# Kernel tuning notes

Hardware: AMD Instinct MI355X
Metric: run time of the kernel (lower is better)

## Reference

```python
import jax, jax.numpy as jnp
import numpy as np

BATCH = 8192
N = 32
A_NUM = 5
EPS = 1e-10
ALPHA = jnp.array([0.01, 0.25, 0.5, 0.9, 0.99], dtype=jnp.float32)


def setup_inputs() -> dict:
    key = jax.random.key(0)
    ks = jax.random.split(key, 9)
    stdv = 1.0 / np.sqrt(N)
    u = lambda k, shape: jax.random.uniform(k, shape, jnp.float32, -stdv, stdv)
    L = N * (N - 1) // 2
    return {
        "inputs": jax.random.normal(ks[0], (BATCH, N, N), jnp.float32),
        "state": jax.random.normal(ks[1], (BATCH, A_NUM * N * N), jnp.float32),
        "WR_root": u(ks[2], (A_NUM,)),
        "Wt_root": u(ks[3], (1,)),
        "Wphi_root": u(ks[4], (1,)),
        "Ws_root": u(ks[5], (A_NUM,)),
        "Br": u(ks[6], (L, 1)),
        "Bt": u(ks[7], (L, 1)),
        "By": u(ks[8], (L, 1)),
    }


def _skew(Bvec, n):
    # Replicates the torch loop: row 0 is zeros; row k (k>=1) gets B[k-1 : 2k-1]
    # in its first k columns (overlapping slices of the flat parameter vector).
    b = Bvec.reshape(-1)
    r = jnp.arange(n)[:, None]
    c = jnp.arange(n)[None, :]
    idx = jnp.clip(r - 1 + c, 0, b.shape[0] - 1)  # B[k-1+j] for entry (k, j)
    L = jnp.where(c < r, b[idx], jnp.zeros((), b.dtype))
    return L - L.T


def _cayley(S, n):
    # MatrixExp in the source: (I - S)^{-1} (I + S)
    I = jnp.eye(n, dtype=S.dtype)
    return jnp.linalg.solve(I - S, I + S)


def _translate(A, Bvec, n):
    # M @ A @ M.T with M the Cayley 'exp' of the skew matrix built from Bvec.
    M = _cayley(_skew(Bvec, n), n)
    return jnp.einsum('ij,bjk,lk->bil', M, A, M)


def _nus(W_root, A, eps):
    # Weighted average over the a_num axis with weights W_root^2 / (sum + eps).
    W = W_root * W_root
    return jnp.einsum('a,banm->bnm', W / (W.sum() + eps), A)


def reference(inputs, state, WR_root, Wt_root, Wphi_root, Ws_root, Br, Bt, By):
    Mt_1 = state.reshape(-1, A_NUM, N, N)                 # [B, a, n, n]
    X = inputs.reshape(BATCH, N, N)                       # [B, n, n]

    Yt = _nus(WR_root, Mt_1, EPS)                         # [B, n, n]
    Rt = _translate(Yt, Br, N)

    at = (Wt_root[0] ** 2) / ((Wt_root ** 2 + Wphi_root ** 2).sum() + EPS)
    Tt = (1.0 - at) * X + at * Rt                         # Frechet mean FM
    Phit = _translate(Tt, Bt, N)

    # Per-j Frechet means, vectorized over the a_num axis.
    a = ALPHA[None, :, None, None]
    Mt = (1.0 - a) * Mt_1 + a * Phit[:, None, :, :]       # [B, a, n, n]

    St = _nus(Ws_root, Mt, EPS)
    Ot = _translate(St, By, N)                            # [B, n, n]

    return Ot, Mt.reshape(-1, A_NUM, N, N)
```

## Files before the change

kernel.cpp:

```cpp
#include <hip/hip_runtime.h>

#define NB 8192
#define OT_ELEMS (NB * 1024)
#define EPSF 1e-10f

typedef __attribute__((ext_vector_type(4))) float f32x4;
typedef __attribute__((ext_vector_type(8))) short s16x8;

#define SBAR() __builtin_amdgcn_sched_barrier(0)
#define LGK()  do { SBAR(); asm volatile("s_waitcnt lgkmcnt(0)"); SBAR(); } while (0)

#define MFMA_B16(A, B, C) __builtin_amdgcn_mfma_f32_16x16x32_bf16((A), (B), (C), 0, 0, 0)

__global__ void cayley_kernel(const float* __restrict__ Br,
                              const float* __restrict__ Bt,
                              const float* __restrict__ By,
                              float* __restrict__ M_out) {
  __shared__ float A[32][33];
  __shared__ float R[32][33];
  const float* B = (blockIdx.x == 0) ? Br : (blockIdx.x == 1) ? Bt : By;
  const int t = threadIdx.x;
  const int i = t >> 5, j = t & 31;
  float Lij = (j < i) ? B[i - 1 + j] : 0.0f;
  float Lji = (i < j) ? B[j - 1 + i] : 0.0f;
  float S = Lij - Lji;
  float eye = (i == j) ? 1.0f : 0.0f;
  A[i][j] = eye - S;
  R[i][j] = eye + S;
  __syncthreads();
  for (int p = 0; p < 32; ++p) {
    float f = A[i][p] / A[p][p];
    __syncthreads();
    if (i != p) {
      A[i][j] -= f * A[p][j];
      R[i][j] -= f * R[p][j];
    }
    __syncthreads();
  }
  M_out[blockIdx.x * 1024 + i * 32 + j] = R[i][j] / A[i][i];
}

__global__ void combine_kernel(float* __restrict__ ws) {
  __shared__ float sMR[1024], sMT[1024];
  const int t = threadIdx.x;
  sMR[t] = ws[t];
  sMT[t] = ws[1024 + t];
  __syncthreads();
  const int i = t >> 5, j = t & 31;
  float s = 0.f;
#pragma unroll
  for (int k = 0; k < 32; ++k)
    s = fmaf(sMT[i * 32 + k], sMR[k * 32 + j], s);
  ws[3072 + i * 32 + j] = s;
}

__device__ __forceinline__ void cvt_hilo8(const f32x4 f0, const f32x4 f1, s16x8& hi, s16x8& lo) {
  float f[8];
#pragma unroll
  for (int e = 0; e < 4; ++e) { f[e] = f0[e]; f[4 + e] = f1[e]; }
#pragma unroll
  for (int e = 0; e < 8; ++e) {
    unsigned u = __float_as_uint(f[e]);
    hi[e] = (short)(u >> 16);
    float ah = __uint_as_float(u & 0xffff0000u);
    lo[e] = (short)(__float_as_uint(f[e] - ah) >> 16);
  }
}

__device__ __forceinline__ void read_frag_lds(const float* sb, int off, s16x8& hi, s16x8& lo) {
  f32x4 f0 = *(const f32x4*)(sb + off);
  f32x4 f1 = *(const f32x4*)(sb + off + 4);
  cvt_hilo8(f0, f1, hi, lo);
}

__global__ __launch_bounds__(64) void spdsru_main(
    const float* __restrict__ X, const float* __restrict__ state,
    const float* __restrict__ WR, const float* __restrict__ Wt,
    const float* __restrict__ Wphi, const float* __restrict__ Ws,
    const float* __restrict__ Mg, float* __restrict__ out) {
  __shared__ __align__(16) float sb0[1184];
  __shared__ __align__(16) float sb1[1184];
  const int lane = threadIdx.x;
  const int l15 = lane & 15, l4 = lane >> 4;
  const int i0 = (lane >> 3) << 2, j0 = (lane & 7) << 2;
  const int bid = blockIdx.x;
  const int batch = (bid & 7) * (NB >> 3) + (bid >> 3);

  s16x8 Mh[3][2], Ml[3][2];
  {
    const int srcoff[3] = {1024, 3072, 2048};
#pragma unroll
    for (int q = 0; q < 3; ++q)
#pragma unroll
      for (int s = 0; s < 2; ++s) {
        const float* p = Mg + srcoff[q] + (16 * s + l15) * 32 + 8 * l4;
        cvt_hilo8(*(const f32x4*)p, *(const f32x4*)(p + 4), Mh[q][s], Ml[q][s]);
      }
  }

  const float alpha[5] = {0.01f, 0.25f, 0.5f, 0.9f, 0.99f};
  float wr[5], va[5];
  float cP = 0.f;
  {
    float sR = 0.f, sS = 0.f, wq[5];
#pragma unroll
    for (int a = 0; a < 5; ++a) { float v = WR[a]; wr[a] = v * v; sR += v * v; }
#pragma unroll
    for (int a = 0; a < 5; ++a) { float v = Ws[a]; wq[a] = v * v; sS += v * v; }
    const float invR = 1.0f / (sR + EPSF), invS = 1.0f / (sS + EPSF);
#pragma unroll
    for (int a = 0; a < 5; ++a) {
      wr[a] *= invR;
      float w = wq[a] * invS;
      va[a] = w * (1.0f - alpha[a]);
      cP += w * alpha[a];
    }
  }
  const float wt2 = Wt[0] * Wt[0], wp2 = Wphi[0] * Wphi[0];
  const float at = wt2 / (wt2 + wp2 + EPSF);
  const float omat = 1.0f - at;

  const float* xp = X + (size_t)batch * 1024;
  f32x4 x[4];
#pragma unroll
  for (int r = 0; r < 4; ++r)
    x[r] = __builtin_nontemporal_load((const f32x4*)(xp + (i0 + r) * 32 + j0));

  const float* stp = state + (size_t)batch * 5120;
  f32x4 U[4], V[4];
#pragma unroll
  for (int r = 0; r < 4; ++r) { U[r] = f32x4{0.f, 0.f, 0.f, 0.f}; V[r] = U[r]; }
#pragma unroll
  for (int a = 0; a < 5; ++a)
#pragma unroll
    for (int r = 0; r < 4; ++r) {
      const f32x4 v = *(const f32x4*)(stp + a * 1024 + (i0 + r) * 32 + j0);
      U[r] += wr[a] * v;
      V[r] += va[a] * v;
    }

#pragma unroll
  for (int c = 0; c < 4; ++c) {
    f32x4 cx = {x[0][c], x[1][c], x[2][c], x[3][c]};
    f32x4 cu = {U[0][c], U[1][c], U[2][c], U[3][c]};
    *(f32x4*)(sb0 + (j0 + c) * 36 + i0) = cx;
    *(f32x4*)(sb1 + (j0 + c) * 36 + i0) = cu;
  }
  LGK();
  s16x8 BXh[2], BXl[2], BUh[2], BUl[2];
#pragma unroll
  for (int s = 0; s < 2; ++s) {
    read_frag_lds(sb0, (16 * s + l15) * 36 + 8 * l4, BXh[s], BXl[s]);
    read_frag_lds(sb1, (16 * s + l15) * 36 + 8 * l4, BUh[s], BUl[s]);
  }
  LGK();
  f32x4 gX[2][2], gU[2][2];
#pragma unroll
  for (int ms = 0; ms < 2; ++ms)
#pragma unroll
    for (int ns = 0; ns < 2; ++ns) {
      f32x4 a0 = {0.f, 0.f, 0.f, 0.f};
      a0 = MFMA_B16(Ml[0][ms], BXh[ns], a0);
      a0 = MFMA_B16(Mh[0][ms], BXl[ns], a0);
      a0 = MFMA_B16(Mh[0][ms], BXh[ns], a0);
      gX[ms][ns] = a0;
      f32x4 a1 = {0.f, 0.f, 0.f, 0.f};
      a1 = MFMA_B16(Ml[1][ms], BUh[ns], a1);
      a1 = MFMA_B16(Mh[1][ms], BUl[ns], a1);
      a1 = MFMA_B16(Mh[1][ms], BUh[ns], a1);
      gU[ms][ns] = a1;
    }
#pragma unroll
  for (int ms = 0; ms < 2; ++ms)
#pragma unroll
    for (int ns = 0; ns < 2; ++ns)
#pragma unroll
      for (int r = 0; r < 4; ++r) {
        sb0[(16 * ms + 4 * l4 + r) * 36 + 16 * ns + l15] = gX[ms][ns][r];
        sb1[(16 * ms + 4 * l4 + r) * 36 + 16 * ns + l15] = gU[ms][ns][r];
      }
  LGK();
  s16x8 AXh[2], AXl[2], AUh[2], AUl[2];
#pragma unroll
  for (int s = 0; s < 2; ++s) {
    read_frag_lds(sb0, (16 * s + l15) * 36 + 8 * l4, AXh[s], AXl[s]);
    read_frag_lds(sb1, (16 * s + l15) * 36 + 8 * l4, AUh[s], AUl[s]);
  }
  LGK();
  f32x4 ph[2][2];
#pragma unroll
  for (int ms = 0; ms < 2; ++ms)
#pragma unroll
    for (int ns = 0; ns < 2; ++ns) {
      f32x4 a0 = {0.f, 0.f, 0.f, 0.f};
      a0 = MFMA_B16(AXl[ms], Mh[0][ns], a0);
      a0 = MFMA_B16(AXh[ms], Ml[0][ns], a0);
      a0 = MFMA_B16(AXh[ms], Mh[0][ns], a0);
      f32x4 a1 = {0.f, 0.f, 0.f, 0.f};
      a1 = MFMA_B16(AUl[ms], Mh[1][ns], a1);
      a1 = MFMA_B16(AUh[ms], Ml[1][ns], a1);
      a1 = MFMA_B16(AUh[ms], Mh[1][ns], a1);
      ph[ms][ns] = omat * a0 + at * a1;
    }

#pragma unroll
  for (int ms = 0; ms < 2; ++ms)
#pragma unroll
    for (int ns = 0; ns < 2; ++ns)
#pragma unroll
      for (int r = 0; r < 4; ++r)
        sb0[(16 * ms + 4 * l4 + r) * 36 + 16 * ns + l15] = ph[ms][ns][r];
  LGK();
  f32x4 ph4[4];
#pragma unroll
  for (int r = 0; r < 4; ++r)
    ph4[r] = *(const f32x4*)(sb0 + (i0 + r) * 36 + j0);
  LGK();

  f32x4 st4[4];
#pragma unroll
  for (int r = 0; r < 4; ++r) st4[r] = V[r] + cP * ph4[r];
#pragma unroll
  for (int c = 0; c < 4; ++c) {
    f32x4 cs = {st4[0][c], st4[1][c], st4[2][c], st4[3][c]};
    *(f32x4*)(sb0 + (j0 + c) * 36 + i0) = cs;
  }
  f32x4 raw[20];
#pragma unroll
  for (int a = 0; a < 5; ++a)
#pragma unroll
    for (int r = 0; r < 4; ++r)
      raw[a * 4 + r] = *(const f32x4*)(stp + a * 1024 + (i0 + r) * 32 + j0);
  LGK();

  s16x8 BSh[2], BSl[2];
#pragma unroll
  for (int s = 0; s < 2; ++s)
    read_frag_lds(sb0, (16 * s + l15) * 36 + 8 * l4, BSh[s], BSl[s]);
  LGK();
  f32x4 gS[2][2];
#pragma unroll
  for (int ms = 0; ms < 2; ++ms)
#pragma unroll
    for (int ns = 0; ns < 2; ++ns) {
      f32x4 acc = {0.f, 0.f, 0.f, 0.f};
      acc = MFMA_B16(Ml[2][ms], BSh[ns], acc);
      acc = MFMA_B16(Mh[2][ms], BSl[ns], acc);
      acc = MFMA_B16(Mh[2][ms], BSh[ns], acc);
      gS[ms][ns] = acc;
    }
  float* outMt = out + OT_ELEMS + (size_t)batch * 5120;
#pragma unroll
  for (int a = 0; a < 5; ++a) {
    const float al = alpha[a], om = 1.0f - al;
#pragma unroll
    for (int r = 0; r < 4; ++r) {
      f32x4 w = om * raw[a * 4 + r] + al * ph4[r];
      __builtin_nontemporal_store(w, (f32x4*)(outMt + a * 1024 + (i0 + r) * 32 + j0));
    }
  }
#pragma unroll
  for (int ms = 0; ms < 2; ++ms)
#pragma unroll
    for (int ns = 0; ns < 2; ++ns)
#pragma unroll
      for (int r = 0; r < 4; ++r)
        sb0[(16 * ms + 4 * l4 + r) * 36 + 16 * ns + l15] = gS[ms][ns][r];
  LGK();
  s16x8 ASh[2], ASl[2];
#pragma unroll
  for (int s = 0; s < 2; ++s)
    read_frag_lds(sb0, (16 * s + l15) * 36 + 8 * l4, ASh[s], ASl[s]);
  LGK();
  f32x4 o[2][2];
#pragma unroll
  for (int ms = 0; ms < 2; ++ms)
#pragma unroll
    for (int ns = 0; ns < 2; ++ns) {
      f32x4 acc = {0.f, 0.f, 0.f, 0.f};
      acc = MFMA_B16(ASl[ms], Mh[2][ns], acc);
      acc = MFMA_B16(ASh[ms], Ml[2][ns], acc);
      acc = MFMA_B16(ASh[ms], Mh[2][ns], acc);
      o[ms][ns] = acc;
    }
#pragma unroll
  for (int ms = 0; ms < 2; ++ms)
#pragma unroll
    for (int ns = 0; ns < 2; ++ns)
#pragma unroll
      for (int r = 0; r < 4; ++r)
        sb0[(16 * ms + 4 * l4 + r) * 36 + 16 * ns + l15] = o[ms][ns][r];
  LGK();
  float* outOt = out + (size_t)batch * 1024;
#pragma unroll
  for (int r = 0; r < 4; ++r) {
    f32x4 ov = *(const f32x4*)(sb0 + (i0 + r) * 36 + j0);
    __builtin_nontemporal_store(ov, (f32x4*)(outOt + (i0 + r) * 32 + j0));
  }
}

extern "C" void kernel_launch(void* const* d_in, const int* in_sizes, int n_in,
                              void* d_out, int out_size, void* d_ws, size_t ws_size,
                              hipStream_t stream) {
  const float* X     = (const float*)d_in[0];
  const float* state = (const float*)d_in[1];
  const float* WR    = (const float*)d_in[2];
  const float* Wt    = (const float*)d_in[3];
  const float* Wphi  = (const float*)d_in[4];
  const float* Ws    = (const float*)d_in[5];
  const float* Br    = (const float*)d_in[6];
  const float* Bt    = (const float*)d_in[7];
  const float* By    = (const float*)d_in[8];
  float* m_ws = (float*)d_ws;
  float* outp = (float*)d_out;

  cayley_kernel<<<3, 1024, 0, stream>>>(Br, Bt, By, m_ws);
  combine_kernel<<<1, 1024, 0, stream>>>(m_ws);
  spdsru_main<<<NB, 64, 0, stream>>>(X, state, WR, Wt, Wphi, Ws, m_ws, outp);
}
```

Baseline: 89.09 us.

## Precompose Cayley matrix products to flatten the dependent matmul chain

The combine kernel now also precomputes My*Mt and My*Mt*Mr, so the final output Ot is expressed directly as My·V·My^T + cP·omat·(MyMt)X(MyMt)^T + cP·at·(MyMtMr)U(...)^T. This removes the serial Phi→St→Ot stage and its LDS round trips, so all five first-stage products can be issued together and then all second-stage products. The state is loaded once into registers and reused for the Mt output instead of being reloaded. In exchange it does more MFMA work (five sandwich products instead of four), uses more LDS buffers and registers (which may lower occupancy), and changes the rounding behaviour of the bf16 hi/lo split.

```diff
diff --git a/kernel.cpp b/kernel.cpp
--- a/kernel.cpp
+++ b/kernel.cpp
@@ -41,17 +41,28 @@
 }
 
 __global__ void combine_kernel(float* __restrict__ ws) {
-  __shared__ float sMR[1024], sMT[1024];
+  __shared__ float sMR[1024], sMT[1024], sMY[1024], sP[1024];
   const int t = threadIdx.x;
   sMR[t] = ws[t];
   sMT[t] = ws[1024 + t];
+  sMY[t] = ws[2048 + t];
   __syncthreads();
   const int i = t >> 5, j = t & 31;
-  float s = 0.f;
+  float p = 0.f, q1 = 0.f;
+#pragma unroll
+  for (int k = 0; k < 32; ++k) {
+    p  = fmaf(sMT[i * 32 + k], sMR[k * 32 + j], p);
+    q1 = fmaf(sMY[i * 32 + k], sMT[k * 32 + j], q1);
+  }
+  sP[i * 32 + j] = p;
+  ws[3072 + i * 32 + j] = p;
+  ws[4096 + i * 32 + j] = q1;
+  __syncthreads();
+  float q2 = 0.f;
 #pragma unroll
   for (int k = 0; k < 32; ++k)
-    s = fmaf(sMT[i * 32 + k], sMR[k * 32 + j], s);
-  ws[3072 + i * 32 + j] = s;
+    q2 = fmaf(sMY[i * 32 + k], sP[k * 32 + j], q2);
+  ws[5120 + i * 32 + j] = q2;
 }
 
 __device__ __forceinline__ void cvt_hilo8(const f32x4 f0, const f32x4 f1, s16x8& hi, s16x8& lo) {
@@ -73,24 +84,30 @@
   cvt_hilo8(f0, f1, hi, lo);
 }
 
+#define PROD3(ACC, MH, ML, BH, BL)             \
+  do {                                         \
+    ACC = MFMA_B16((ML), (BH), ACC);           \
+    ACC = MFMA_B16((MH), (BL), ACC);           \
+    ACC = MFMA_B16((MH), (BH), ACC);           \
+  } while (0)
+
 __global__ __launch_bounds__(64) void spdsru_main(
     const float* __restrict__ X, const float* __restrict__ state,
     const float* __restrict__ WR, const float* __restrict__ Wt,
     const float* __restrict__ Wphi, const float* __restrict__ Ws,
     const float* __restrict__ Mg, float* __restrict__ out) {
-  __shared__ __align__(16) float sb0[1184];
-  __shared__ __align__(16) float sb1[1184];
+  __shared__ __align__(16) float sb0[1184], sb1[1184], sb2[1184], sb3[1184], sb4[1184];
   const int lane = threadIdx.x;
   const int l15 = lane & 15, l4 = lane >> 4;
   const int i0 = (lane >> 3) << 2, j0 = (lane & 7) << 2;
   const int bid = blockIdx.x;
   const int batch = (bid & 7) * (NB >> 3) + (bid >> 3);
 
-  s16x8 Mh[3][2], Ml[3][2];
+  s16x8 Mh[5][2], Ml[5][2];
   {
-    const int srcoff[3] = {1024, 3072, 2048};
-#pragma unroll
-    for (int q = 0; q < 3; ++q)
+    const int srcoff[5] = {1024, 3072, 2048, 4096, 5120};
+#pragma unroll
+    for (int q = 0; q < 5; ++q)
 #pragma unroll
       for (int s = 0; s < 2; ++s) {
         const float* p = Mg + srcoff[q] + (16 * s + l15) * 32 + 8 * l4;
@@ -119,184 +136,151 @@
   const float wt2 = Wt[0] * Wt[0], wp2 = Wphi[0] * Wphi[0];
   const float at = wt2 / (wt2 + wp2 + EPSF);
   const float omat = 1.0f - at;
-
+  const float cpo = cP * omat, cpa = cP * at;
+
+  const float* stp = state + (size_t)batch * 5120;
+  f32x4 m[5][4];
+#pragma unroll
+  for (int a = 0; a < 5; ++a)
+#pragma unroll
+    for (int r = 0; r < 4; ++r)
+      m[a][r] = *(const f32x4*)(stp + a * 1024 + (i0 + r) * 32 + j0);
   const float* xp = X + (size_t)batch * 1024;
   f32x4 x[4];
 #pragma unroll
   for (int r = 0; r < 4; ++r)
     x[r] = __builtin_nontemporal_load((const f32x4*)(xp + (i0 + r) * 32 + j0));
 
-  const float* stp = state + (size_t)batch * 5120;
   f32x4 U[4], V[4];
 #pragma unroll
-  for (int r = 0; r < 4; ++r) { U[r] = f32x4{0.f, 0.f, 0.f, 0.f}; V[r] = U[r]; }
-#pragma unroll
-  for (int a = 0; a < 5; ++a)
-#pragma unroll
-    for (int r = 0; r < 4; ++r) {
-      const f32x4 v = *(const f32x4*)(stp + a * 1024 + (i0 + r) * 32 + j0);
-      U[r] += wr[a] * v;
-      V[r] += va[a] * v;
-    }
+  for (int r = 0; r < 4; ++r) {
+    f32x4 u = wr[0] * m[0][r], v = va[0] * m[0][r];
+#pragma unroll
+    for (int a = 1; a < 5; ++a) { u += wr[a] * m[a][r]; v += va[a] * m[a][r]; }
+    U[r] = u; V[r] = v;
+  }
 
 #pragma unroll
   for (int c = 0; c < 4; ++c) {
     f32x4 cx = {x[0][c], x[1][c], x[2][c], x[3][c]};
     f32x4 cu = {U[0][c], U[1][c], U[2][c], U[3][c]};
+    f32x4 cv = {V[0][c], V[1][c], V[2][c], V[3][c]};
     *(f32x4*)(sb0 + (j0 + c) * 36 + i0) = cx;
     *(f32x4*)(sb1 + (j0 + c) * 36 + i0) = cu;
-  }
-  LGK();
-  s16x8 BXh[2], BXl[2], BUh[2], BUl[2];
+    *(f32x4*)(sb2 + (j0 + c) * 36 + i0) = cv;
+  }
+  LGK();
+
+  s16x8 BXh[2], BXl[2], BUh[2], BUl[2], BVh[2], BVl[2];
 #pragma unroll
   for (int s = 0; s < 2; ++s) {
     read_frag_lds(sb0, (16 * s + l15) * 36 + 8 * l4, BXh[s], BXl[s]);
     read_frag_lds(sb1, (16 * s + l15) * 36 + 8 * l4, BUh[s], BUl[s]);
-  }
-  LGK();
-  f32x4 gX[2][2], gU[2][2];
+    read_frag_lds(sb2, (16 * s + l15) * 36 + 8 * l4, BVh[s], BVl[s]);
+  }
+  LGK();
+
+#define STAGE_G(SB, G)                                                      \
+  do {                                                                      \
+    _Pragma("unroll") for (int ms = 0; ms < 2; ++ms)                        \
+      _Pragma("unroll") for (int ns = 0; ns < 2; ++ns)                      \
+        _Pragma("unroll") for (int r = 0; r < 4; ++r)                       \
+          (SB)[(16 * ms + 4 * l4 + r) * 36 + 16 * ns + l15] = G[ms][ns][r]; \
+  } while (0)
+
+  {
+    f32x4 g[2][2];
+#pragma unroll
+    for (int ms = 0; ms < 2; ++ms)
+#pragma unroll
+      for (int ns = 0; ns < 2; ++ns) { f32x4 a = {0,0,0,0}; PROD3(a, Mh[0][ms], Ml[0][ms], BXh[ns], BXl[ns]); g[ms][ns] = a; }
+    STAGE_G(sb0, g);
+#pragma unroll
+    for (int ms = 0; ms < 2; ++ms)
+#pragma unroll
+      for (int ns = 0; ns < 2; ++ns) { f32x4 a = {0,0,0,0}; PROD3(a, Mh[1][ms], Ml[1][ms], BUh[ns], BUl[ns]); g[ms][ns] = a; }
+    STAGE_G(sb1, g);
+#pragma unroll
+    for (int ms = 0; ms < 2; ++ms)
+#pragma unroll
+      for (int ns = 0; ns < 2; ++ns) { f32x4 a = {0,0,0,0}; PROD3(a, Mh[2][ms], Ml[2][ms], BVh[ns], BVl[ns]); g[ms][ns] = a; }
+    STAGE_G(sb2, g);
+#pragma unroll
+    for (int ms = 0; ms < 2; ++ms)
+#pragma unroll
+      for (int ns = 0; ns < 2; ++ns) { f32x4 a = {0,0,0,0}; PROD3(a, Mh[3][ms], Ml[3][ms], BXh[ns], BXl[ns]); g[ms][ns] = a; }
+    STAGE_G(sb3, g);
+#pragma unroll
+    for (int ms = 0; ms < 2; ++ms)
+#pragma unroll
+      for (int ns = 0; ns < 2; ++ns) { f32x4 a = {0,0,0,0}; PROD3(a, Mh[4][ms], Ml[4][ms], BUh[ns], BUl[ns]); g[ms][ns] = a; }
+    STAGE_G(sb4, g);
+  }
+  LGK();
+
+  s16x8 A1h[2], A1l[2], A2h[2], A2l[2];
+#pragma unroll
+  for (int s = 0; s < 2; ++s) {
+    read_frag_lds(sb0, (16 * s + l15) * 36 + 8 * l4, A1h[s], A1l[s]);
+    read_frag_lds(sb1, (16 * s + l15) * 36 + 8 * l4, A2h[s], A2l[s]);
+  }
+  LGK();
+
+  f32x4 ph[2][2];
 #pragma unroll
   for (int ms = 0; ms < 2; ++ms)
 #pragma unroll
     for (int ns = 0; ns < 2; ++ns) {
-      f32x4 a0 = {0.f, 0.f, 0.f, 0.f};
-      a0 = MFMA_B16(Ml[0][ms], BXh[ns], a0);
-      a0 = MFMA_B16(Mh[0][ms], BXl[ns], a0);
-      a0 = MFMA_B16(Mh[0][ms], BXh[ns], a0);
-      gX[ms][ns] = a0;
-      f32x4 a1 = {0.f, 0.f, 0.f, 0.f};
-      a1 = MFMA_B16(Ml[1][ms], BUh[ns], a1);
-      a1 = MFMA_B16(Mh[1][ms], BUl[ns], a1);
-      a1 = MFMA_B16(Mh[1][ms], BUh[ns], a1);
-      gU[ms][ns] = a1;
-    }
+      f32x4 a0 = {0,0,0,0}, a1 = {0,0,0,0};
+      PROD3(a0, A1h[ms], A1l[ms], Mh[0][ns], Ml[0][ns]);
+      PROD3(a1, A2h[ms], A2l[ms], Mh[1][ns], Ml[1][ns]);
+      ph[ms][ns] = omat * a0 + at * a1;
+    }
+  s16x8 A3h[2], A3l[2], A4h[2], A4l[2], A5h[2], A5l[2];
+#pragma unroll
+  for (int s = 0; s < 2; ++s) {
+    read_frag_lds(sb2, (16 * s + l15) * 36 + 8 * l4, A3h[s], A3l[s]);
+    read_frag_lds(sb3, (16 * s + l15) * 36 + 8 * l4, A4h[s], A4l[s]);
+    read_frag_lds(sb4, (16 * s + l15) * 36 + 8 * l4, A5h[s], A5l[s]);
+  }
+  LGK();
+
+  f32x4 ot[2][2];
 #pragma unroll
   for (int ms = 0; ms < 2; ++ms)
 #pragma unroll
-    for (int ns = 0; ns < 2; ++ns)
-#pragma unroll
-      for (int r = 0; r < 4; ++r) {
-        sb0[(16 * ms + 4 * l4 + r) * 36 + 16 * ns + l15] = gX[ms][ns][r];
-        sb1[(16 * ms + 4 * l4 + r) * 36 + 16 * ns + l15] = gU[ms][ns][r];
-      }
-  LGK();
-  s16x8 AXh[2], AXl[2], AUh[2], AUl[2];
-#pragma unroll
-  for (int s = 0; s < 2; ++s) {
-    read_frag_lds(sb0, (16 * s + l15) * 36 + 8 * l4, AXh[s], AXl[s]);
-    read_frag_lds(sb1, (16 * s + l15) * 36 + 8 * l4, AUh[s], AUl[s]);
-  }
-  LGK();
-  f32x4 ph[2][2];
-#pragma unroll
-  for (int ms = 0; ms < 2; ++ms)
-#pragma unroll
     for (int ns = 0; ns < 2; ++ns) {
-      f32x4 a0 = {0.f, 0.f, 0.f, 0.f};
-      a0 = MFMA_B16(AXl[ms], Mh[0][ns], a0);
-      a0 = MFMA_B16(AXh[ms], Ml[0][ns], a0);
-      a0 = MFMA_B16(AXh[ms], Mh[0][ns], a0);
-      f32x4 a1 = {0.f, 0.f, 0.f, 0.f};
-      a1 = MFMA_B16(AUl[ms], Mh[1][ns], a1);
-      a1 = MFMA_B16(AUh[ms], Ml[1][ns], a1);
-      a1 = MFMA_B16(AUh[ms], Mh[1][ns], a1);
-      ph[ms][ns] = omat * a0 + at * a1;
-    }
-
-#pragma unroll
-  for (int ms = 0; ms < 2; ++ms)
-#pragma unroll
-    for (int ns = 0; ns < 2; ++ns)
-#pragma unroll
-      for (int r = 0; r < 4; ++r)
-        sb0[(16 * ms + 4 * l4 + r) * 36 + 16 * ns + l15] = ph[ms][ns][r];
-  LGK();
-  f32x4 ph4[4];
-#pragma unroll
-  for (int r = 0; r < 4; ++r)
+      f32x4 a0 = {0,0,0,0}, a1 = {0,0,0,0}, a2 = {0,0,0,0};
+      PROD3(a0, A3h[ms], A3l[ms], Mh[2][ns], Ml[2][ns]);
+      PROD3(a1, A4h[ms], A4l[ms], Mh[3][ns], Ml[3][ns]);
+      PROD3(a2, A5h[ms], A5l[ms], Mh[4][ns], Ml[4][ns]);
+      ot[ms][ns] = a0 + cpo * a1 + cpa * a2;
+    }
+  STAGE_G(sb0, ph);
+  STAGE_G(sb1, ot);
+  LGK();
+
+  f32x4 ph4[4], ot4[4];
+#pragma unroll
+  for (int r = 0; r < 4; ++r) {
     ph4[r] = *(const f32x4*)(sb0 + (i0 + r) * 36 + j0);
-  LGK();
-
-  f32x4 st4[4];
-#pragma unroll
-  for (int r = 0; r < 4; ++r) st4[r] = V[r] + cP * ph4[r];
-#pragma unroll
-  for (int c = 0; c < 4; ++c) {
-    f32x4 cs = {st4[0][c], st4[1][c], st4[2][c], st4[3][c]};
-    *(f32x4*)(sb0 + (j0 + c) * 36 + i0) = cs;
-  }
-  f32x4 raw[20];
-#pragma unroll
-  for (int a = 0; a < 5; ++a)
-#pragma unroll
-    for (int r = 0; r < 4; ++r)
-      raw[a * 4 + r] = *(const f32x4*)(stp + a * 1024 + (i0 + r) * 32 + j0);
-  LGK();
-
-  s16x8 BSh[2], BSl[2];
-#pragma unroll
-  for (int s = 0; s < 2; ++s)
-    read_frag_lds(sb0, (16 * s + l15) * 36 + 8 * l4, BSh[s], BSl[s]);
-  LGK();
-  f32x4 gS[2][2];
-#pragma unroll
-  for (int ms = 0; ms < 2; ++ms)
-#pragma unroll
-    for (int ns = 0; ns < 2; ++ns) {
-      f32x4 acc = {0.f, 0.f, 0.f, 0.f};
-      acc = MFMA_B16(Ml[2][ms], BSh[ns], acc);
-      acc = MFMA_B16(Mh[2][ms], BSl[ns], acc);
-      acc = MFMA_B16(Mh[2][ms], BSh[ns], acc);
-      gS[ms][ns] = acc;
-    }
+    ot4[r] = *(const f32x4*)(sb1 + (i0 + r) * 36 + j0);
+  }
   float* outMt = out + OT_ELEMS + (size_t)batch * 5120;
 #pragma unroll
   for (int a = 0; a < 5; ++a) {
     const float al = alpha[a], om = 1.0f - al;
 #pragma unroll
     for (int r = 0; r < 4; ++r) {
-      f32x4 w = om * raw[a * 4 + r] + al * ph4[r];
+      f32x4 w = om * m[a][r] + al * ph4[r];
       __builtin_nontemporal_store(w, (f32x4*)(outMt + a * 1024 + (i0 + r) * 32 + j0));
     }
   }
-#pragma unroll
-  for (int ms = 0; ms < 2; ++ms)
-#pragma unroll
-    for (int ns = 0; ns < 2; ++ns)
-#pragma unroll
-      for (int r = 0; r < 4; ++r)
-        sb0[(16 * ms + 4 * l4 + r) * 36 + 16 * ns + l15] = gS[ms][ns][r];
-  LGK();
-  s16x8 ASh[2], ASl[2];
-#pragma unroll
-  for (int s = 0; s < 2; ++s)
-    read_frag_lds(sb0, (16 * s + l15) * 36 + 8 * l4, ASh[s], ASl[s]);
-  LGK();
-  f32x4 o[2][2];
-#pragma unroll
-  for (int ms = 0; ms < 2; ++ms)
-#pragma unroll
-    for (int ns = 0; ns < 2; ++ns) {
-      f32x4 acc = {0.f, 0.f, 0.f, 0.f};
-      acc = MFMA_B16(ASl[ms], Mh[2][ns], acc);
-      acc = MFMA_B16(ASh[ms], Ml[2][ns], acc);
-      acc = MFMA_B16(ASh[ms], Mh[2][ns], acc);
-      o[ms][ns] = acc;
-    }
-#pragma unroll
-  for (int ms = 0; ms < 2; ++ms)
-#pragma unroll
-    for (int ns = 0; ns < 2; ++ns)
-#pragma unroll
-      for (int r = 0; r < 4; ++r)
-        sb0[(16 * ms + 4 * l4 + r) * 36 + 16 * ns + l15] = o[ms][ns][r];
-  LGK();
   float* outOt = out + (size_t)batch * 1024;
 #pragma unroll
-  for (int r = 0; r < 4; ++r) {
-    f32x4 ov = *(const f32x4*)(sb0 + (i0 + r) * 36 + j0);
-    __builtin_nontemporal_store(ov, (f32x4*)(outOt + (i0 + r) * 32 + j0));
-  }
+  for (int r = 0; r < 4; ++r)
+    __builtin_nontemporal_store(ot4[r], (f32x4*)(outOt + (i0 + r) * 32 + j0));
+#undef STAGE_G
 }
 
 extern "C" void kernel_launch(void* const* d_in, const int* in_sizes, int n_in,
```

Measured after the change: 91.91 us. 1.03x slower.

## Hoist global loads to kernel start and stagger X/U translate chains

Applied to the files above, without the earlier changes.

Issues the X and state loads at the very beginning, before the weight-matrix conversion and scalar setup, so global memory latency overlaps that work. The X-side translate now starts before the weighted state sum is reduced, and the second X GEMM is interleaved with the first U GEMM, which overlaps LDS round-trips with MFMA work. The risk is much higher register pressure from keeping 20 raw state vectors live across the early stages. The state is still reloaded later for the Mt output, so global traffic does not drop.

```diff
diff --git a/kernel.cpp b/kernel.cpp
--- a/kernel.cpp
+++ b/kernel.cpp
@@ -86,6 +86,20 @@
   const int bid = blockIdx.x;
   const int batch = (bid & 7) * (NB >> 3) + (bid >> 3);
 
+  const float* xp = X + (size_t)batch * 1024;
+  f32x4 x[4];
+#pragma unroll
+  for (int r = 0; r < 4; ++r)
+    x[r] = __builtin_nontemporal_load((const f32x4*)(xp + (i0 + r) * 32 + j0));
+
+  const float* stp = state + (size_t)batch * 5120;
+  f32x4 raw[20];
+#pragma unroll
+  for (int a = 0; a < 5; ++a)
+#pragma unroll
+    for (int r = 0; r < 4; ++r)
+      raw[a * 4 + r] = *(const f32x4*)(stp + a * 1024 + (i0 + r) * 32 + j0);
+
   s16x8 Mh[3][2], Ml[3][2];
   {
     const int srcoff[3] = {1024, 3072, 2048};
@@ -120,41 +134,20 @@
   const float at = wt2 / (wt2 + wp2 + EPSF);
   const float omat = 1.0f - at;
 
-  const float* xp = X + (size_t)batch * 1024;
-  f32x4 x[4];
-#pragma unroll
-  for (int r = 0; r < 4; ++r)
-    x[r] = __builtin_nontemporal_load((const f32x4*)(xp + (i0 + r) * 32 + j0));
-
-  const float* stp = state + (size_t)batch * 5120;
-  f32x4 U[4], V[4];
-#pragma unroll
-  for (int r = 0; r < 4; ++r) { U[r] = f32x4{0.f, 0.f, 0.f, 0.f}; V[r] = U[r]; }
-#pragma unroll
-  for (int a = 0; a < 5; ++a)
-#pragma unroll
-    for (int r = 0; r < 4; ++r) {
-      const f32x4 v = *(const f32x4*)(stp + a * 1024 + (i0 + r) * 32 + j0);
-      U[r] += wr[a] * v;
-      V[r] += va[a] * v;
-    }
-
 #pragma unroll
   for (int c = 0; c < 4; ++c) {
     f32x4 cx = {x[0][c], x[1][c], x[2][c], x[3][c]};
-    f32x4 cu = {U[0][c], U[1][c], U[2][c], U[3][c]};
     *(f32x4*)(sb0 + (j0 + c) * 36 + i0) = cx;
-    *(f32x4*)(sb1 + (j0 + c) * 36 + i0) = cu;
-  }
-  LGK();
-  s16x8 BXh[2], BXl[2], BUh[2], BUl[2];
-#pragma unroll
-  for (int s = 0; s < 2; ++s) {
+  }
+  LGK();
+
+  s16x8 BXh[2], BXl[2];
+#pragma unroll
+  for (int s = 0; s < 2; ++s)
     read_frag_lds(sb0, (16 * s + l15) * 36 + 8 * l4, BXh[s], BXl[s]);
-    read_frag_lds(sb1, (16 * s + l15) * 36 + 8 * l4, BUh[s], BUl[s]);
-  }
-  LGK();
-  f32x4 gX[2][2], gU[2][2];
+  LGK();
+
+  f32x4 gX[2][2];
 #pragma unroll
   for (int ms = 0; ms < 2; ++ms)
 #pragma unroll
@@ -164,6 +157,47 @@
       a0 = MFMA_B16(Mh[0][ms], BXl[ns], a0);
       a0 = MFMA_B16(Mh[0][ms], BXh[ns], a0);
       gX[ms][ns] = a0;
+    }
+#pragma unroll
+  for (int ms = 0; ms < 2; ++ms)
+#pragma unroll
+    for (int ns = 0; ns < 2; ++ns)
+#pragma unroll
+      for (int r = 0; r < 4; ++r)
+        sb0[(16 * ms + 4 * l4 + r) * 36 + 16 * ns + l15] = gX[ms][ns][r];
+  f32x4 U[4], V[4];
+#pragma unroll
+  for (int r = 0; r < 4; ++r) {
+    f32x4 u = wr[0] * raw[r], v = va[0] * raw[r];
+#pragma unroll
+    for (int a = 1; a < 5; ++a) { u += wr[a] * raw[a * 4 + r]; v += va[a] * raw[a * 4 + r]; }
+    U[r] = u; V[r] = v;
+  }
+#pragma unroll
+  for (int c = 0; c < 4; ++c) {
+    f32x4 cu = {U[0][c], U[1][c], U[2][c], U[3][c]};
+    *(f32x4*)(sb1 + (j0 + c) * 36 + i0) = cu;
+  }
+  LGK();
+
+  s16x8 AXh[2], AXl[2], BUh[2], BUl[2];
+#pragma unroll
+  for (int s = 0; s < 2; ++s) {
+    read_frag_lds(sb0, (16 * s + l15) * 36 + 8 * l4, AXh[s], AXl[s]);
+    read_frag_lds(sb1, (16 * s + l15) * 36 + 8 * l4, BUh[s], BUl[s]);
+  }
+  LGK();
+
+  f32x4 a0c[2][2], gU[2][2];
+#pragma unroll
+  for (int ms = 0; ms < 2; ++ms)
+#pragma unroll
+    for (int ns = 0; ns < 2; ++ns) {
+      f32x4 a0 = {0.f, 0.f, 0.f, 0.f};
+      a0 = MFMA_B16(AXl[ms], Mh[0][ns], a0);
+      a0 = MFMA_B16(AXh[ms], Ml[0][ns], a0);
+      a0 = MFMA_B16(AXh[ms], Mh[0][ns], a0);
+      a0c[ms][ns] = a0;
       f32x4 a1 = {0.f, 0.f, 0.f, 0.f};
       a1 = MFMA_B16(Ml[1][ms], BUh[ns], a1);
       a1 = MFMA_B16(Mh[1][ms], BUl[ns], a1);
@@ -175,34 +209,27 @@
 #pragma unroll
     for (int ns = 0; ns < 2; ++ns)
 #pragma unroll
-      for (int r = 0; r < 4; ++r) {
-        sb0[(16 * ms + 4 * l4 + r) * 36 + 16 * ns + l15] = gX[ms][ns][r];
+      for (int r = 0; r < 4; ++r)
         sb1[(16 * ms + 4 * l4 + r) * 36 + 16 * ns + l15] = gU[ms][ns][r];
-      }
-  LGK();
-  s16x8 AXh[2], AXl[2], AUh[2], AUl[2];
-#pragma unroll
-  for (int s = 0; s < 2; ++s) {
-    read_frag_lds(sb0, (16 * s + l15) * 36 + 8 * l4, AXh[s], AXl[s]);
+  LGK();
+
+  s16x8 AUh[2], AUl[2];
+#pragma unroll
+  for (int s = 0; s < 2; ++s)
     read_frag_lds(sb1, (16 * s + l15) * 36 + 8 * l4, AUh[s], AUl[s]);
-  }
-  LGK();
+  LGK();
+
   f32x4 ph[2][2];
 #pragma unroll
   for (int ms = 0; ms < 2; ++ms)
 #pragma unroll
     for (int ns = 0; ns < 2; ++ns) {
-      f32x4 a0 = {0.f, 0.f, 0.f, 0.f};
-      a0 = MFMA_B16(AXl[ms], Mh[0][ns], a0);
-      a0 = MFMA_B16(AXh[ms], Ml[0][ns], a0);
-      a0 = MFMA_B16(AXh[ms], Mh[0][ns], a0);
       f32x4 a1 = {0.f, 0.f, 0.f, 0.f};
       a1 = MFMA_B16(AUl[ms], Mh[1][ns], a1);
       a1 = MFMA_B16(AUh[ms], Ml[1][ns], a1);
       a1 = MFMA_B16(AUh[ms], Mh[1][ns], a1);
-      ph[ms][ns] = omat * a0 + at * a1;
-    }
-
+      ph[ms][ns] = omat * a0c[ms][ns] + at * a1;
+    }
 #pragma unroll
   for (int ms = 0; ms < 2; ++ms)
 #pragma unroll
@@ -211,6 +238,7 @@
       for (int r = 0; r < 4; ++r)
         sb0[(16 * ms + 4 * l4 + r) * 36 + 16 * ns + l15] = ph[ms][ns][r];
   LGK();
+
   f32x4 ph4[4];
 #pragma unroll
   for (int r = 0; r < 4; ++r)
@@ -225,12 +253,12 @@
     f32x4 cs = {st4[0][c], st4[1][c], st4[2][c], st4[3][c]};
     *(f32x4*)(sb0 + (j0 + c) * 36 + i0) = cs;
   }
-  f32x4 raw[20];
+  f32x4 raw2[20];
 #pragma unroll
   for (int a = 0; a < 5; ++a)
 #pragma unroll
     for (int r = 0; r < 4; ++r)
-      raw[a * 4 + r] = *(const f32x4*)(stp + a * 1024 + (i0 + r) * 32 + j0);
+      raw2[a * 4 + r] = *(const f32x4*)(stp + a * 1024 + (i0 + r) * 32 + j0);
   LGK();
 
   s16x8 BSh[2], BSl[2];
@@ -238,6 +266,7 @@
   for (int s = 0; s < 2; ++s)
     read_frag_lds(sb0, (16 * s + l15) * 36 + 8 * l4, BSh[s], BSl[s]);
   LGK();
+
   f32x4 gS[2][2];
 #pragma unroll
   for (int ms = 0; ms < 2; ++ms)
@@ -255,7 +284,7 @@
     const float al = alpha[a], om = 1.0f - al;
 #pragma unroll
     for (int r = 0; r < 4; ++r) {
-      f32x4 w = om * raw[a * 4 + r] + al * ph4[r];
+      f32x4 w = om * raw2[a * 4 + r] + al * ph4[r];
       __builtin_nontemporal_store(w, (f32x4*)(outMt + a * 1024 + (i0 + r) * 32 + j0));
     }
   }
@@ -267,11 +296,13 @@
       for (int r = 0; r < 4; ++r)
         sb0[(16 * ms + 4 * l4 + r) * 36 + 16 * ns + l15] = gS[ms][ns][r];
   LGK();
+
   s16x8 ASh[2], ASl[2];
 #pragma unroll
   for (int s = 0; s < 2; ++s)
     read_frag_lds(sb0, (16 * s + l15) * 36 + 8 * l4, ASh[s], ASl[s]);
   LGK();
+
   f32x4 o[2][2];
 #pragma unroll
   for (int ms = 0; ms < 2; ++ms)
@@ -291,6 +322,7 @@
       for (int r = 0; r < 4; ++r)
         sb0[(16 * ms + 4 * l4 + r) * 36 + 16 * ns + l15] = o[ms][ns][r];
   LGK();
+
   float* outOt = out + (size_t)batch * 1024;
 #pragma unroll
   for (int r = 0; r < 4; ++r) {
```

Result: slower. 92.25 us (+3.5%).

## Process two batches per block with async global-to-LDS state prefetch

Applied to the files above, without the earlier changes.

Each 64-thread block now handles two batch elements instead of one, halving the grid. The 20 KB state slab is loaded straight into LDS with global_load_lds, and the second batch's state is prefetched while the first batch is being computed. State values are reread from LDS for the Mt output instead of being held in 20 registers. The LDS footprint per block grows to about 50 KB, which limits how many blocks fit per CU. The vmcnt(0) wait also stalls on every outstanding load, so latency hiding depends on the larger tiles.

```diff
diff --git a/kernel.cpp b/kernel.cpp
--- a/kernel.cpp
+++ b/kernel.cpp
@@ -9,6 +9,7 @@
 
 #define SBAR() __builtin_amdgcn_sched_barrier(0)
 #define LGK()  do { SBAR(); asm volatile("s_waitcnt lgkmcnt(0)"); SBAR(); } while (0)
+#define VMC0() do { SBAR(); asm volatile("s_waitcnt vmcnt(0)"); SBAR(); } while (0)
 
 #define MFMA_B16(A, B, C) __builtin_amdgcn_mfma_f32_16x16x32_bf16((A), (B), (C), 0, 0, 0)
 
@@ -73,6 +74,18 @@
   cvt_hilo8(f0, f1, hi, lo);
 }
 
+__device__ __forceinline__ void gload_lds16(const float* g, float* l) {
+  __builtin_amdgcn_global_load_lds(
+      (const __attribute__((address_space(1))) unsigned*)(g),
+      (__attribute__((address_space(3))) unsigned*)(l), 16, 0, 0);
+}
+
+__device__ __forceinline__ void issue_state(const float* g, float* l, int lane) {
+#pragma unroll
+  for (int k = 0; k < 20; ++k)
+    gload_lds16(g + k * 256 + lane * 4, l + k * 256);
+}
+
 __global__ __launch_bounds__(64) void spdsru_main(
     const float* __restrict__ X, const float* __restrict__ state,
     const float* __restrict__ WR, const float* __restrict__ Wt,
@@ -80,11 +93,15 @@
     const float* __restrict__ Mg, float* __restrict__ out) {
   __shared__ __align__(16) float sb0[1184];
   __shared__ __align__(16) float sb1[1184];
+  __shared__ __align__(16) float sstA[5120];
+  __shared__ __align__(16) float sstB[5120];
   const int lane = threadIdx.x;
   const int l15 = lane & 15, l4 = lane >> 4;
   const int i0 = (lane >> 3) << 2, j0 = (lane & 7) << 2;
   const int bid = blockIdx.x;
-  const int batch = (bid & 7) * (NB >> 3) + (bid >> 3);
+  const int batch0 = (((bid & 7) * ((NB / 2) >> 3)) + (bid >> 3)) * 2;
+
+  issue_state(state + (size_t)batch0 * 5120, sstA, lane);
 
   s16x8 Mh[3][2], Ml[3][2];
   {
@@ -120,182 +137,197 @@
   const float at = wt2 / (wt2 + wp2 + EPSF);
   const float omat = 1.0f - at;
 
-  const float* xp = X + (size_t)batch * 1024;
-  f32x4 x[4];
-#pragma unroll
-  for (int r = 0; r < 4; ++r)
-    x[r] = __builtin_nontemporal_load((const f32x4*)(xp + (i0 + r) * 32 + j0));
-
-  const float* stp = state + (size_t)batch * 5120;
-  f32x4 U[4], V[4];
-#pragma unroll
-  for (int r = 0; r < 4; ++r) { U[r] = f32x4{0.f, 0.f, 0.f, 0.f}; V[r] = U[r]; }
-#pragma unroll
-  for (int a = 0; a < 5; ++a)
+#pragma unroll
+  for (int g = 0; g < 2; ++g) {
+    float* sst = g ? sstB : sstA;
+    const int batch = batch0 + g;
+
+    const float* xp = X + (size_t)batch * 1024;
+    f32x4 x[4];
+#pragma unroll
+    for (int r = 0; r < 4; ++r)
+      x[r] = __builtin_nontemporal_load((const f32x4*)(xp + (i0 + r) * 32 + j0));
+
+    VMC0();
+
+    f32x4 U[4], V[4];
+#pragma unroll
+    for (int r = 0; r < 4; ++r) { U[r] = f32x4{0.f, 0.f, 0.f, 0.f}; V[r] = U[r]; }
+#pragma unroll
+    for (int a = 0; a < 5; ++a)
+#pragma unroll
+      for (int r = 0; r < 4; ++r) {
+        const f32x4 v = *(const f32x4*)(sst + a * 1024 + (i0 + r) * 32 + j0);
+        U[r] += wr[a] * v;
+        V[r] += va[a] * v;
+      }
+
+    if (g == 0)
+      issue_state(state + (size_t)(batch0 + 1) * 5120, sstB, lane);
+#pragma unroll
+    for (int c = 0; c < 4; ++c) {
+      f32x4 cx = {x[0][c], x[1][c], x[2][c], x[3][c]};
+      f32x4 cu = {U[0][c], U[1][c], U[2][c], U[3][c]};
+      *(f32x4*)(sb0 + (j0 + c) * 36 + i0) = cx;
+      *(f32x4*)(sb1 + (j0 + c) * 36 + i0) = cu;
+    }
+    LGK();
+
+    s16x8 BXh[2], BXl[2], BUh[2], BUl[2];
+#pragma unroll
+    for (int s = 0; s < 2; ++s) {
+      read_frag_lds(sb0, (16 * s + l15) * 36 + 8 * l4, BXh[s], BXl[s]);
+      read_frag_lds(sb1, (16 * s + l15) * 36 + 8 * l4, BUh[s], BUl[s]);
+    }
+    LGK();
+
+    f32x4 gX[2][2], gU[2][2];
+#pragma unroll
+    for (int ms = 0; ms < 2; ++ms)
+#pragma unroll
+      for (int ns = 0; ns < 2; ++ns) {
+        f32x4 a0 = {0.f, 0.f, 0.f, 0.f};
+        a0 = MFMA_B16(Ml[0][ms], BXh[ns], a0);
+        a0 = MFMA_B16(Mh[0][ms], BXl[ns], a0);
+        a0 = MFMA_B16(Mh[0][ms], BXh[ns], a0);
+        gX[ms][ns] = a0;
+        f32x4 a1 = {0.f, 0.f, 0.f, 0.f};
+        a1 = MFMA_B16(Ml[1][ms], BUh[ns], a1);
+        a1 = MFMA_B16(Mh[1][ms], BUl[ns], a1);
+        a1 = MFMA_B16(Mh[1][ms], BUh[ns], a1);
+        gU[ms][ns] = a1;
+      }
+#pragma unroll
+    for (int ms = 0; ms < 2; ++ms)
+#pragma unroll
+      for (int ns = 0; ns < 2; ++ns)
+#pragma unroll
+        for (int r = 0; r < 4; ++r) {
+          sb0[(16 * ms + 4 * l4 + r) * 36 + 16 * ns + l15] = gX[ms][ns][r];
+          sb1[(16 * ms + 4 * l4 + r) * 36 + 16 * ns + l15] = gU[ms][ns][r];
+        }
+    LGK();
+
+    s16x8 AXh[2], AXl[2], AUh[2], AUl[2];
+#pragma unroll
+    for (int s = 0; s < 2; ++s) {
+      read_frag_lds(sb0, (16 * s + l15) * 36 + 8 * l4, AXh[s], AXl[s]);
+      read_frag_lds(sb1, (16 * s + l15) * 36 + 8 * l4, AUh[s], AUl[s]);
+    }
+    LGK();
+
+    f32x4 ph[2][2];
+#pragma unroll
+    for (int ms = 0; ms < 2; ++ms)
+#pragma unroll
+      for (int ns = 0; ns < 2; ++ns) {
+        f32x4 a0 = {0.f, 0.f, 0.f, 0.f};
+        a0 = MFMA_B16(AXl[ms], Mh[0][ns], a0);
+        a0 = MFMA_B16(AXh[ms], Ml[0][ns], a0);
+        a0 = MFMA_B16(AXh[ms], Mh[0][ns], a0);
+        f32x4 a1 = {0.f, 0.f, 0.f, 0.f};
+        a1 = MFMA_B16(AUl[ms], Mh[1][ns], a1);
+        a1 = MFMA_B16(AUh[ms], Ml[1][ns], a1);
+        a1 = MFMA_B16(AUh[ms], Mh[1][ns], a1);
+        ph[ms][ns] = omat * a0 + at * a1;
+      }
+#pragma unroll
+    for (int ms = 0; ms < 2; ++ms)
+#pragma unroll
+      for (int ns = 0; ns < 2; ++ns)
+#pragma unroll
+        for (int r = 0; r < 4; ++r)
+          sb0[(16 * ms + 4 * l4 + r) * 36 + 16 * ns + l15] = ph[ms][ns][r];
+    LGK();
+
+    f32x4 ph4[4];
+#pragma unroll
+    for (int r = 0; r < 4; ++r)
+      ph4[r] = *(const f32x4*)(sb0 + (i0 + r) * 36 + j0);
+    LGK();
+
+    f32x4 st4[4];
+#pragma unroll
+    for (int r = 0; r < 4; ++r) st4[r] = V[r] + cP * ph4[r];
+#pragma unroll
+    for (int c = 0; c < 4; ++c) {
+      f32x4 cs = {st4[0][c], st4[1][c], st4[2][c], st4[3][c]};
+      *(f32x4*)(sb0 + (j0 + c) * 36 + i0) = cs;
+    }
+    LGK();
+
+    s16x8 BSh[2], BSl[2];
+#pragma unroll
+    for (int s = 0; s < 2; ++s)
+      read_frag_lds(sb0, (16 * s + l15) * 36 + 8 * l4, BSh[s], BSl[s]);
+    LGK();
+
+    f32x4 gS[2][2];
+#pragma unroll
+    for (int ms = 0; ms < 2; ++ms)
+#pragma unroll
+      for (int ns = 0; ns < 2; ++ns) {
+        f32x4 acc = {0.f, 0.f, 0.f, 0.f};
+        acc = MFMA_B16(Ml[2][ms], BSh[ns], acc);
+        acc = MFMA_B16(Mh[2][ms], BSl[ns], acc);
+        acc = MFMA_B16(Mh[2][ms], BSh[ns], acc);
+        gS[ms][ns] = acc;
+      }
+    {
+      float* outMt = out + OT_ELEMS + (size_t)batch * 5120;
+#pragma unroll
+      for (int a = 0; a < 5; ++a) {
+        const float al = alpha[a], om = 1.0f - al;
+#pragma unroll
+        for (int r = 0; r < 4; ++r) {
+          const f32x4 v = *(const f32x4*)(sst + a * 1024 + (i0 + r) * 32 + j0);
+          f32x4 w = om * v + al * ph4[r];
+          __builtin_nontemporal_store(w, (f32x4*)(outMt + a * 1024 + (i0 + r) * 32 + j0));
+        }
+      }
+    }
+#pragma unroll
+    for (int ms = 0; ms < 2; ++ms)
+#pragma unroll
+      for (int ns = 0; ns < 2; ++ns)
+#pragma unroll
+        for (int r = 0; r < 4; ++r)
+          sb0[(16 * ms + 4 * l4 + r) * 36 + 16 * ns + l15] = gS[ms][ns][r];
+    LGK();
+
+    s16x8 ASh[2], ASl[2];
+#pragma unroll
+    for (int s = 0; s < 2; ++s)
+      read_frag_lds(sb0, (16 * s + l15) * 36 + 8 * l4, ASh[s], ASl[s]);
+    LGK();
+
+    f32x4 o[2][2];
+#pragma unroll
+    for (int ms = 0; ms < 2; ++ms)
+#pragma unroll
+      for (int ns = 0; ns < 2; ++ns) {
+        f32x4 acc = {0.f, 0.f, 0.f, 0.f};
+        acc = MFMA_B16(ASl[ms], Mh[2][ns], acc);
+        acc = MFMA_B16(ASh[ms], Ml[2][ns], acc);
+        acc = MFMA_B16(ASh[ms], Mh[2][ns], acc);
+        o[ms][ns] = acc;
+      }
+#pragma unroll
+    for (int ms = 0; ms < 2; ++ms)
+#pragma unroll
+      for (int ns = 0; ns < 2; ++ns)
+#pragma unroll
+        for (int r = 0; r < 4; ++r)
+          sb0[(16 * ms + 4 * l4 + r) * 36 + 16 * ns + l15] = o[ms][ns][r];
+    LGK();
+
+    float* outOt = out + (size_t)batch * 1024;
 #pragma unroll
     for (int r = 0; r < 4; ++r) {
-      const f32x4 v = *(const f32x4*)(stp + a * 1024 + (i0 + r) * 32 + j0);
-      U[r] += wr[a] * v;
-      V[r] += va[a] * v;
-    }
-
-#pragma unroll
-  for (int c = 0; c < 4; ++c) {
-    f32x4 cx = {x[0][c], x[1][c], x[2][c], x[3][c]};
-    f32x4 cu = {U[0][c], U[1][c], U[2][c], U[3][c]};
-    *(f32x4*)(sb0 + (j0 + c) * 36 + i0) = cx;
-    *(f32x4*)(sb1 + (j0 + c) * 36 + i0) = cu;
-  }
-  LGK();
-  s16x8 BXh[2], BXl[2], BUh[2], BUl[2];
-#pragma unroll
-  for (int s = 0; s < 2; ++s) {
-    read_frag_lds(sb0, (16 * s + l15) * 36 + 8 * l4, BXh[s], BXl[s]);
-    read_frag_lds(sb1, (16 * s + l15) * 36 + 8 * l4, BUh[s], BUl[s]);
-  }
-  LGK();
-  f32x4 gX[2][2], gU[2][2];
-#pragma unroll
-  for (int ms = 0; ms < 2; ++ms)
-#pragma unroll
-    for (int ns = 0; ns < 2; ++ns) {
-      f32x4 a0 = {0.f, 0.f, 0.f, 0.f};
-      a0 = MFMA_B16(Ml[0][ms], BXh[ns], a0);
-      a0 = MFMA_B16(Mh[0][ms], BXl[ns], a0);
-      a0 = MFMA_B16(Mh[0][ms], BXh[ns], a0);
-      gX[ms][ns] = a0;
-      f32x4 a1 = {0.f, 0.f, 0.f, 0.f};
-      a1 = MFMA_B16(Ml[1][ms], BUh[ns], a1);
-      a1 = MFMA_B16(Mh[1][ms], BUl[ns], a1);
-      a1 = MFMA_B16(Mh[1][ms], BUh[ns], a1);
-      gU[ms][ns] = a1;
-    }
-#pragma unroll
-  for (int ms = 0; ms < 2; ++ms)
-#pragma unroll
-    for (int ns = 0; ns < 2; ++ns)
-#pragma unroll
-      for (int r = 0; r < 4; ++r) {
-        sb0[(16 * ms + 4 * l4 + r) * 36 + 16 * ns + l15] = gX[ms][ns][r];
-        sb1[(16 * ms + 4 * l4 + r) * 36 + 16 * ns + l15] = gU[ms][ns][r];
-      }
-  LGK();
-  s16x8 AXh[2], AXl[2], AUh[2], AUl[2];
-#pragma unroll
-  for (int s = 0; s < 2; ++s) {
-    read_frag_lds(sb0, (16 * s + l15) * 36 + 8 * l4, AXh[s], AXl[s]);
-    read_frag_lds(sb1, (16 * s + l15) * 36 + 8 * l4, AUh[s], AUl[s]);
-  }
-  LGK();
-  f32x4 ph[2][2];
-#pragma unroll
-  for (int ms = 0; ms < 2; ++ms)
-#pragma unroll
-    for (int ns = 0; ns < 2; ++ns) {
-      f32x4 a0 = {0.f, 0.f, 0.f, 0.f};
-      a0 = MFMA_B16(AXl[ms], Mh[0][ns], a0);
-      a0 = MFMA_B16(AXh[ms], Ml[0][ns], a0);
-      a0 = MFMA_B16(AXh[ms], Mh[0][ns], a0);
-      f32x4 a1 = {0.f, 0.f, 0.f, 0.f};
-      a1 = MFMA_B16(AUl[ms], Mh[1][ns], a1);
-      a1 = MFMA_B16(AUh[ms], Ml[1][ns], a1);
-      a1 = MFMA_B16(AUh[ms], Mh[1][ns], a1);
-      ph[ms][ns] = omat * a0 + at * a1;
-    }
-
-#pragma unroll
-  for (int ms = 0; ms < 2; ++ms)
-#pragma unroll
-    for (int ns = 0; ns < 2; ++ns)
-#pragma unroll
-      for (int r = 0; r < 4; ++r)
-        sb0[(16 * ms + 4 * l4 + r) * 36 + 16 * ns + l15] = ph[ms][ns][r];
-  LGK();
-  f32x4 ph4[4];
-#pragma unroll
-  for (int r = 0; r < 4; ++r)
-    ph4[r] = *(const f32x4*)(sb0 + (i0 + r) * 36 + j0);
-  LGK();
-
-  f32x4 st4[4];
-#pragma unroll
-  for (int r = 0; r < 4; ++r) st4[r] = V[r] + cP * ph4[r];
-#pragma unroll
-  for (int c = 0; c < 4; ++c) {
-    f32x4 cs = {st4[0][c], st4[1][c], st4[2][c], st4[3][c]};
-    *(f32x4*)(sb0 + (j0 + c) * 36 + i0) = cs;
-  }
-  f32x4 raw[20];
-#pragma unroll
-  for (int a = 0; a < 5; ++a)
-#pragma unroll
-    for (int r = 0; r < 4; ++r)
-      raw[a * 4 + r] = *(const f32x4*)(stp + a * 1024 + (i0 + r) * 32 + j0);
-  LGK();
-
-  s16x8 BSh[2], BSl[2];
-#pragma unroll
-  for (int s = 0; s < 2; ++s)
-    read_frag_lds(sb0, (16 * s + l15) * 36 + 8 * l4, BSh[s], BSl[s]);
-  LGK();
-  f32x4 gS[2][2];
-#pragma unroll
-  for (int ms = 0; ms < 2; ++ms)
-#pragma unroll
-    for (int ns = 0; ns < 2; ++ns) {
-      f32x4 acc = {0.f, 0.f, 0.f, 0.f};
-      acc = MFMA_B16(Ml[2][ms], BSh[ns], acc);
-      acc = MFMA_B16(Mh[2][ms], BSl[ns], acc);
-      acc = MFMA_B16(Mh[2][ms], BSh[ns], acc);
-      gS[ms][ns] = acc;
-    }
-  float* outMt = out + OT_ELEMS + (size_t)batch * 5120;
-#pragma unroll
-  for (int a = 0; a < 5; ++a) {
-    const float al = alpha[a], om = 1.0f - al;
-#pragma unroll
-    for (int r = 0; r < 4; ++r) {
-      f32x4 w = om * raw[a * 4 + r] + al * ph4[r];
-      __builtin_nontemporal_store(w, (f32x4*)(outMt + a * 1024 + (i0 + r) * 32 + j0));
-    }
-  }
-#pragma unroll
-  for (int ms = 0; ms < 2; ++ms)
-#pragma unroll
-    for (int ns = 0; ns < 2; ++ns)
-#pragma unroll
-      for (int r = 0; r < 4; ++r)
-        sb0[(16 * ms + 4 * l4 + r) * 36 + 16 * ns + l15] = gS[ms][ns][r];
-  LGK();
-  s16x8 ASh[2], ASl[2];
-#pragma unroll
-  for (int s = 0; s < 2; ++s)
-    read_frag_lds(sb0, (16 * s + l15) * 36 + 8 * l4, ASh[s], ASl[s]);
-  LGK();
-  f32x4 o[2][2];
-#pragma unroll
-  for (int ms = 0; ms < 2; ++ms)
-#pragma unroll
-    for (int ns = 0; ns < 2; ++ns) {
-      f32x4 acc = {0.f, 0.f, 0.f, 0.f};
-      acc = MFMA_B16(ASl[ms], Mh[2][ns], acc);
-      acc = MFMA_B16(ASh[ms], Ml[2][ns], acc);
-      acc = MFMA_B16(ASh[ms], Mh[2][ns], acc);
-      o[ms][ns] = acc;
-    }
-#pragma unroll
-  for (int ms = 0; ms < 2; ++ms)
-#pragma unroll
-    for (int ns = 0; ns < 2; ++ns)
-#pragma unroll
-      for (int r = 0; r < 4; ++r)
-        sb0[(16 * ms + 4 * l4 + r) * 36 + 16 * ns + l15] = o[ms][ns][r];
-  LGK();
-  float* outOt = out + (size_t)batch * 1024;
-#pragma unroll
-  for (int r = 0; r < 4; ++r) {
-    f32x4 ov = *(const f32x4*)(sb0 + (i0 + r) * 36 + j0);
-    __builtin_nontemporal_store(ov, (f32x4*)(outOt + (i0 + r) * 32 + j0));
+      f32x4 ov = *(const f32x4*)(sb0 + (i0 + r) * 36 + j0);
+      __builtin_nontemporal_store(ov, (f32x4*)(outOt + (i0 + r) * 32 + j0));
+    }
+    LGK();
   }
 }
 
@@ -316,5 +348,5 @@
 
   cayley_kernel<<<3, 1024, 0, stream>>>(Br, Bt, By, m_ws);
   combine_kernel<<<1, 1024, 0, stream>>>(m_ws);
-  spdsru_main<<<NB, 64, 0, stream>>>(X, state, WR, Wt, Wphi, Ws, m_ws, outp);
-}
+  spdsru_main<<<NB / 2, 64, 0, stream>>>(X, state, WR, Wt, Wphi, Ws, m_ws, outp);
+}
```

New measurement: 99.67 us. 11.9% more time.
